# Kernel optimization log

Measured on AMD Instinct MI355X. Metric: run time of the kernel, lower is better.

## Reference

```python
import jax, jax.numpy as jnp
import numpy as np

B, H, N, C = 1024, 768, 100000, 42
LABELED_WEIGHT = 0.7
NUM_LABELED = 100000  # used verbatim in (1 - num_labeled) per the original source
EPS = 1e-8  # F.cosine_similarity default eps


def setup_inputs() -> dict:
    key = jax.random.key(0)
    k1, k2, k3, k4 = jax.random.split(key, 4)
    return {
        "weak_data": jax.random.normal(k1, (B, H), dtype=jnp.float32),
        "weak_logits": jax.random.normal(k2, (B, C), dtype=jnp.float32),
        "labeled_memory": jax.random.normal(k3, (N, H), dtype=jnp.float32),
        "labeled_logits": jax.random.normal(k4, (N, C), dtype=jnp.float32),
    }


def reference(weak_data, weak_logits, labeled_memory, labeled_logits):
    # cosine similarity: normalize rows with eps-clamped norms, then one GEMM
    dn = weak_data / jnp.maximum(jnp.linalg.norm(weak_data, axis=-1, keepdims=True), EPS)
    mn = labeled_memory / jnp.maximum(jnp.linalg.norm(labeled_memory, axis=-1, keepdims=True), EPS)
    sim = jnp.einsum("bh,nh->bn", dn, mn)  # [B, N] similarity (the large intermediate)
    ids = jnp.argmax(sim, axis=1)          # 1-NN index per batch row
    batch_logits = labeled_logits[ids]     # gather [B, C]
    # faithful to source: coefficient is (1 - num_labeled), as written in update_logits
    return batch_logits * LABELED_WEIGHT + (1.0 - NUM_LABELED) * weak_logits
```

## Files before the change

kernel.cpp:

```cpp
#include <hip/hip_runtime.h>
#include <stdint.h>

#define B_ROWS 1024
#define H_DIM  768
#define N_ROWS 100000
#define C_DIM  42
#define NB     64
#define NCHUNK ((N_ROWS + NB - 1) / NB)
#define K2_BLOCKS 782
#define K2_THREADS 512

typedef __attribute__((ext_vector_type(8))) short short8;
typedef __attribute__((ext_vector_type(4))) float f32x4;

__device__ __forceinline__ unsigned short f2bf(float f) {
    union { float f; unsigned u; } x; x.f = f;
    unsigned r = x.u + 0x7FFFu + ((x.u >> 16) & 1u);
    return (unsigned short)(r >> 16);
}

__device__ __forceinline__ unsigned long long packvi(float v, unsigned n) {
    unsigned u = __float_as_uint(v);
    u = (u & 0x80000000u) ? ~u : (u | 0x80000000u);
    return ((unsigned long long)u << 32) | (unsigned long long)(~n);
}

__global__ void k_convA(const float* __restrict__ wd, unsigned short* __restrict__ A) {
    int idx = blockIdx.x * 256 + threadIdx.x;
    float4 v = reinterpret_cast<const float4*>(wd)[idx];
    union { unsigned short s[4]; uint2 u; } o;
    o.s[0] = f2bf(v.x); o.s[1] = f2bf(v.y); o.s[2] = f2bf(v.z); o.s[3] = f2bf(v.w);
    reinterpret_cast<uint2*>(A)[idx] = o.u;
}

__global__ __launch_bounds__(512, 2) void k_simmax(
    const float* __restrict__ mem,
    const unsigned short* __restrict__ A,
    unsigned long long* __restrict__ partial)
{
    __shared__ __align__(16) char ldsB[NB * 1536];
    __shared__ float ldsN[NB];

    const int t    = threadIdx.x;
    const int lane = t & 63;
    const int wv   = t >> 6;
    const int fr   = lane & 15;
    const int kgrp = lane >> 4;

    for (int ci = 0; ci < 2; ++ci) {
        const int c = blockIdx.x + ci * K2_BLOCKS;
        if (c >= NCHUNK) break;
        if (ci) __syncthreads();

        {
            const int r  = t >> 3;
            const int cb = (t & 7) * 4;
            const int n  = c * NB + r;
            const bool valid = (n < N_ROWS);
            const float* src = mem + (long long)n * H_DIM + cb;
            char* dst = ldsB + r * 1536;
            const int sw = (r & 7) << 4;
            float ss = 0.f;
            #pragma unroll
            for (int i = 0; i < 24; ++i) {
                float4 v;
                if (valid) v = *reinterpret_cast<const float4*>(src + i * 32);
                else       v = make_float4(0.f, 0.f, 0.f, 0.f);
                ss += v.x*v.x + v.y*v.y + v.z*v.z + v.w*v.w;
                union { unsigned short s[4]; uint2 u; } o;
                o.s[0]=f2bf(v.x); o.s[1]=f2bf(v.y); o.s[2]=f2bf(v.z); o.s[3]=f2bf(v.w);
                int off = (cb + i * 32) * 2;
                *reinterpret_cast<uint2*>(dst + (off ^ sw)) = o.u;
            }
            ss += __shfl_xor(ss, 1);
            ss += __shfl_xor(ss, 2);
            ss += __shfl_xor(ss, 4);
            if ((t & 7) == 0)
                ldsN[r] = valid ? (1.0f / fmaxf(sqrtf(ss), 1e-8f)) : 0.0f;
        }
        __syncthreads();

        float invn[4];
        #pragma unroll
        for (int nt = 0; nt < 4; ++nt) invn[nt] = ldsN[nt * 16 + fr];

        #pragma unroll
        for (int gi = 0; gi < 2; ++gi) {
            const int b0 = (wv + 8 * gi) * 64;
            f32x4 acc[4][4];
            #pragma unroll
            for (int m = 0; m < 4; ++m)
                #pragma unroll
                for (int n = 0; n < 4; ++n)
                    acc[m][n] = (f32x4){0.f, 0.f, 0.f, 0.f};

            #pragma unroll 4
            for (int k = 0; k < 24; ++k) {
                const int k0 = k * 32 + kgrp * 8;
                short8 af[4], bf[4];
                #pragma unroll
                for (int m = 0; m < 4; ++m) {
                    const unsigned short* ap = A + (b0 + m * 16 + fr) * H_DIM + k0;
                    af[m] = *reinterpret_cast<const short8*>(ap);
                }
                #pragma unroll
                for (int n = 0; n < 4; ++n) {
                    int roww = n * 16 + fr;
                    int off  = roww * 1536 + k0 * 2;
                    off ^= (roww & 7) << 4;
                    bf[n] = *reinterpret_cast<const short8*>(ldsB + off);
                }
                #pragma unroll
                for (int m = 0; m < 4; ++m)
                    #pragma unroll
                    for (int n = 0; n < 4; ++n)
                        acc[m][n] = __builtin_amdgcn_mfma_f32_16x16x32_bf16(af[m], bf[n], acc[m][n], 0, 0, 0);
            }

            #pragma unroll
            for (int m = 0; m < 4; ++m) {
                #pragma unroll
                for (int r = 0; r < 4; ++r) {
                    unsigned long long best = 0ull;
                    #pragma unroll
                    for (int nt = 0; nt < 4; ++nt) {
                        unsigned nglob = (unsigned)(c * NB + nt * 16 + fr);
                        float v = acc[m][nt][r] * invn[nt];
                        unsigned long long p = (nglob < N_ROWS) ? packvi(v, nglob) : 0ull;
                        best = (p > best) ? p : best;
                    }
                    #pragma unroll
                    for (int s = 1; s < 16; s <<= 1) {
                        unsigned long long o = __shfl_xor(best, s);
                        best = (o > best) ? o : best;
                    }
                    if (fr == 0) {
                        int brow = b0 + m * 16 + kgrp * 4 + r;
                        partial[(long long)c * 1024 + brow] = best;
                    }
                }
            }
        }
    }
}

__global__ void k_final(const unsigned long long* __restrict__ partial,
                        const float* __restrict__ wlog,
                        const float* __restrict__ llog,
                        float* __restrict__ out)
{
    __shared__ unsigned long long red[16][17];
    __shared__ int sidx[16];
    const int t  = threadIdx.x;
    const int b0 = blockIdx.x * 16;
    const int i  = t >> 4, j = t & 15;

    unsigned long long best = 0ull;
    for (int c = j; c < NCHUNK; c += 16) {
        unsigned long long p = partial[(long long)c * 1024 + b0 + i];
        best = (p > best) ? p : best;
    }
    red[i][j] = best;
    __syncthreads();
    if (t < 16) {
        unsigned long long m = red[t][0];
        #pragma unroll
        for (int jj = 1; jj < 16; ++jj) { unsigned long long p = red[t][jj]; m = (p > m) ? p : m; }
        sidx[t] = (int)(~(unsigned)(m & 0xFFFFFFFFull));
    }
    __syncthreads();
    for (int e = t; e < 16 * C_DIM; e += 256) {
        int bi = e / C_DIM, cc = e % C_DIM;
        int b  = b0 + bi;
        out[b * C_DIM + cc] = 0.7f * llog[(long long)sidx[bi] * C_DIM + cc]
                            - 99999.0f * wlog[b * C_DIM + cc];
    }
}

extern "C" void kernel_launch(void* const* d_in, const int* in_sizes, int n_in,
                              void* d_out, int out_size, void* d_ws, size_t ws_size,
                              hipStream_t stream) {
    const float* weak_data   = (const float*)d_in[0];
    const float* weak_logits = (const float*)d_in[1];
    const float* mem         = (const float*)d_in[2];
    const float* llog        = (const float*)d_in[3];
    float* out = (float*)d_out;

    unsigned short*     A       = (unsigned short*)d_ws;
    unsigned long long* partial = (unsigned long long*)((char*)d_ws + (2u << 20));

    k_convA <<<768, 256, 0, stream>>>(weak_data, A);
    k_simmax<<<K2_BLOCKS, K2_THREADS, 0, stream>>>(mem, A, partial);
    k_final <<<64, 256, 0, stream>>>(partial, weak_logits, llog, out);
}
```

Measured before the change: 922.8 us.

## Use persistent atomic work queue with register-resident argmax and pre-tiled A layout

Result: faster. 901.6 us (-2.3%).

```diff
diff --git a/kernel.cpp b/kernel.cpp
--- a/kernel.cpp
+++ b/kernel.cpp
@@ -5,10 +5,9 @@
 #define H_DIM  768
 #define N_ROWS 100000
 #define C_DIM  42
-#define NB     64
-#define NCHUNK ((N_ROWS + NB - 1) / NB)
-#define K2_BLOCKS 782
-#define K2_THREADS 512
+#define NB     32
+#define NCHUNK (N_ROWS / NB)
+#define GX     384
 
 typedef __attribute__((ext_vector_type(8))) short short8;
 typedef __attribute__((ext_vector_type(4))) float f32x4;
@@ -25,123 +24,143 @@
     return ((unsigned long long)u << 32) | (unsigned long long)(~n);
 }
 
-__global__ void k_convA(const float* __restrict__ wd, unsigned short* __restrict__ A) {
+__global__ void k_convA(const float* __restrict__ wd, unsigned short* __restrict__ A2,
+                        unsigned int* __restrict__ counters) {
+    if (blockIdx.x == 0 && threadIdx.x == 0) { counters[0] = 0; counters[1] = 0; }
     int idx = blockIdx.x * 256 + threadIdx.x;
+    int row = idx / 192;
+    int c4  = idx - row * 192;
+    int col = c4 * 4;
     float4 v = reinterpret_cast<const float4*>(wd)[idx];
     union { unsigned short s[4]; uint2 u; } o;
     o.s[0] = f2bf(v.x); o.s[1] = f2bf(v.y); o.s[2] = f2bf(v.z); o.s[3] = f2bf(v.w);
-    reinterpret_cast<uint2*>(A)[idx] = o.u;
-}
-
-__global__ __launch_bounds__(512, 2) void k_simmax(
+    size_t byte = (size_t)(((row >> 4) * 96 + (col >> 3)) * 256 + (row & 15) * 16 + (col & 7) * 2);
+    *reinterpret_cast<uint2*>((char*)A2 + byte) = o.u;
+}
+
+__global__ __launch_bounds__(256, 3) void k_simmax(
     const float* __restrict__ mem,
-    const unsigned short* __restrict__ A,
+    const unsigned short* __restrict__ A2,
+    unsigned int* __restrict__ counters,
     unsigned long long* __restrict__ partial)
 {
     __shared__ __align__(16) char ldsB[NB * 1536];
     __shared__ float ldsN[NB];
+    __shared__ int s_c;
 
     const int t    = threadIdx.x;
     const int lane = t & 63;
     const int wv   = t >> 6;
     const int fr   = lane & 15;
     const int kgrp = lane >> 4;
-
-    for (int ci = 0; ci < 2; ++ci) {
-        const int c = blockIdx.x + ci * K2_BLOCKS;
+    const int y    = blockIdx.y;
+
+    float    bv[2][4][4];
+    unsigned bi[2][4][4];
+    #pragma unroll
+    for (int gi = 0; gi < 2; ++gi)
+        #pragma unroll
+        for (int m = 0; m < 4; ++m)
+            #pragma unroll
+            for (int r = 0; r < 4; ++r) { bv[gi][m][r] = -1e30f; bi[gi][m][r] = 0u; }
+
+    const char* A2c = (const char*)A2 + (size_t)lane * 16;
+
+    while (true) {
+        __syncthreads();
+        if (t == 0) s_c = (int)atomicAdd(&counters[y], 1u);
+        __syncthreads();
+        const int c = s_c;
         if (c >= NCHUNK) break;
-        if (ci) __syncthreads();
 
         {
             const int r  = t >> 3;
-            const int cb = (t & 7) * 4;
-            const int n  = c * NB + r;
-            const bool valid = (n < N_ROWS);
-            const float* src = mem + (long long)n * H_DIM + cb;
+            const int j  = t & 7;
+            const float* src = mem + (c * NB + r) * H_DIM + j * 4;
             char* dst = ldsB + r * 1536;
             const int sw = (r & 7) << 4;
             float ss = 0.f;
             #pragma unroll
             for (int i = 0; i < 24; ++i) {
-                float4 v;
-                if (valid) v = *reinterpret_cast<const float4*>(src + i * 32);
-                else       v = make_float4(0.f, 0.f, 0.f, 0.f);
+                float4 v = *reinterpret_cast<const float4*>(src + i * 32);
                 ss += v.x*v.x + v.y*v.y + v.z*v.z + v.w*v.w;
                 union { unsigned short s[4]; uint2 u; } o;
                 o.s[0]=f2bf(v.x); o.s[1]=f2bf(v.y); o.s[2]=f2bf(v.z); o.s[3]=f2bf(v.w);
-                int off = (cb + i * 32) * 2;
-                *reinterpret_cast<uint2*>(dst + (off ^ sw)) = o.u;
+                *reinterpret_cast<uint2*>(dst + ((j * 8 + i * 64) ^ sw)) = o.u;
             }
             ss += __shfl_xor(ss, 1);
             ss += __shfl_xor(ss, 2);
             ss += __shfl_xor(ss, 4);
-            if ((t & 7) == 0)
-                ldsN[r] = valid ? (1.0f / fmaxf(sqrtf(ss), 1e-8f)) : 0.0f;
+            if (j == 0) ldsN[r] = 1.0f / fmaxf(sqrtf(ss), 1e-8f);
         }
         __syncthreads();
 
-        float invn[4];
-        #pragma unroll
-        for (int nt = 0; nt < 4; ++nt) invn[nt] = ldsN[nt * 16 + fr];
+        const float invn[2] = { ldsN[fr], ldsN[16 + fr] };
 
         #pragma unroll
         for (int gi = 0; gi < 2; ++gi) {
-            const int b0 = (wv + 8 * gi) * 64;
-            f32x4 acc[4][4];
+            const int rg0 = y * 32 + gi * 16 + wv * 4;
+            const char* ap = A2c + (size_t)rg0 * 24576;
+            f32x4 acc[4][2];
             #pragma unroll
             for (int m = 0; m < 4; ++m)
                 #pragma unroll
-                for (int n = 0; n < 4; ++n)
-                    acc[m][n] = (f32x4){0.f, 0.f, 0.f, 0.f};
-
-            #pragma unroll 4
+                for (int nt = 0; nt < 2; ++nt)
+                    acc[m][nt] = (f32x4){0.f, 0.f, 0.f, 0.f};
+
+            #pragma unroll 6
             for (int k = 0; k < 24; ++k) {
-                const int k0 = k * 32 + kgrp * 8;
-                short8 af[4], bf[4];
-                #pragma unroll
-                for (int m = 0; m < 4; ++m) {
-                    const unsigned short* ap = A + (b0 + m * 16 + fr) * H_DIM + k0;
-                    af[m] = *reinterpret_cast<const short8*>(ap);
-                }
-                #pragma unroll
-                for (int n = 0; n < 4; ++n) {
-                    int roww = n * 16 + fr;
-                    int off  = roww * 1536 + k0 * 2;
-                    off ^= (roww & 7) << 4;
-                    bf[n] = *reinterpret_cast<const short8*>(ldsB + off);
+                short8 af[4], bfr[2];
+                #pragma unroll
+                for (int m = 0; m < 4; ++m)
+                    af[m] = *reinterpret_cast<const short8*>(ap + m * 24576 + k * 1024);
+                #pragma unroll
+                for (int nt = 0; nt < 2; ++nt) {
+                    int roww = nt * 16 + fr;
+                    int off  = (roww * 1536 + k * 64 + kgrp * 16) ^ ((roww & 7) << 4);
+                    bfr[nt] = *reinterpret_cast<const short8*>(ldsB + off);
                 }
                 #pragma unroll
                 for (int m = 0; m < 4; ++m)
                     #pragma unroll
-                    for (int n = 0; n < 4; ++n)
-                        acc[m][n] = __builtin_amdgcn_mfma_f32_16x16x32_bf16(af[m], bf[n], acc[m][n], 0, 0, 0);
-            }
-
-            #pragma unroll
-            for (int m = 0; m < 4; ++m) {
-                #pragma unroll
-                for (int r = 0; r < 4; ++r) {
-                    unsigned long long best = 0ull;
+                    for (int nt = 0; nt < 2; ++nt)
+                        acc[m][nt] = __builtin_amdgcn_mfma_f32_16x16x32_bf16(af[m], bfr[nt], acc[m][nt], 0, 0, 0);
+            }
+
+            const unsigned nb0 = (unsigned)(c * NB) + (unsigned)fr;
+            #pragma unroll
+            for (int nt = 0; nt < 2; ++nt) {
+                const unsigned nv = nb0 + nt * 16;
+                #pragma unroll
+                for (int m = 0; m < 4; ++m)
                     #pragma unroll
-                    for (int nt = 0; nt < 4; ++nt) {
-                        unsigned nglob = (unsigned)(c * NB + nt * 16 + fr);
+                    for (int r = 0; r < 4; ++r) {
                         float v = acc[m][nt][r] * invn[nt];
-                        unsigned long long p = (nglob < N_ROWS) ? packvi(v, nglob) : 0ull;
-                        best = (p > best) ? p : best;
+                        bool p = v > bv[gi][m][r];
+                        bv[gi][m][r] = p ? v : bv[gi][m][r];
+                        bi[gi][m][r] = p ? nv : bi[gi][m][r];
                     }
-                    #pragma unroll
-                    for (int s = 1; s < 16; s <<= 1) {
-                        unsigned long long o = __shfl_xor(best, s);
-                        best = (o > best) ? o : best;
-                    }
-                    if (fr == 0) {
-                        int brow = b0 + m * 16 + kgrp * 4 + r;
-                        partial[(long long)c * 1024 + brow] = best;
-                    }
+            }
+        }
+    }
+
+    #pragma unroll
+    for (int gi = 0; gi < 2; ++gi)
+        #pragma unroll
+        for (int m = 0; m < 4; ++m)
+            #pragma unroll
+            for (int r = 0; r < 4; ++r) {
+                unsigned long long P = packvi(bv[gi][m][r], bi[gi][m][r]);
+                #pragma unroll
+                for (int s = 1; s < 16; s <<= 1) {
+                    unsigned long long o = __shfl_xor(P, s);
+                    P = (o > P) ? o : P;
                 }
-            }
-        }
-    }
+                if (fr == 0) {
+                    int lb = gi * 256 + wv * 64 + m * 16 + kgrp * 4 + r;
+                    partial[((size_t)y * GX + blockIdx.x) * 512 + lb] = P;
+                }
+            }
 }
 
 __global__ void k_final(const unsigned long long* __restrict__ partial,
@@ -149,31 +168,33 @@
                         const float* __restrict__ llog,
                         float* __restrict__ out)
 {
-    __shared__ unsigned long long red[16][17];
     __shared__ int sidx[16];
     const int t  = threadIdx.x;
     const int b0 = blockIdx.x * 16;
     const int i  = t >> 4, j = t & 15;
 
-    unsigned long long best = 0ull;
-    for (int c = j; c < NCHUNK; c += 16) {
-        unsigned long long p = partial[(long long)c * 1024 + b0 + i];
-        best = (p > best) ? p : best;
-    }
-    red[i][j] = best;
+    const int b  = b0 + i;
+    const int yy = b >> 9;
+    const int lb = b & 511;
+
+    unsigned long long P = 0ull;
+    for (int g = j; g < GX; g += 16) {
+        unsigned long long p = partial[((size_t)yy * GX + g) * 512 + lb];
+        P = (p > P) ? p : P;
+    }
+    #pragma unroll
+    for (int s = 1; s < 16; s <<= 1) {
+        unsigned long long o = __shfl_xor(P, s);
+        P = (o > P) ? o : P;
+    }
+    if (j == 0) sidx[i] = (int)(~(unsigned)(P & 0xFFFFFFFFull));
     __syncthreads();
-    if (t < 16) {
-        unsigned long long m = red[t][0];
-        #pragma unroll
-        for (int jj = 1; jj < 16; ++jj) { unsigned long long p = red[t][jj]; m = (p > m) ? p : m; }
-        sidx[t] = (int)(~(unsigned)(m & 0xFFFFFFFFull));
-    }
-    __syncthreads();
+
     for (int e = t; e < 16 * C_DIM; e += 256) {
-        int bi = e / C_DIM, cc = e % C_DIM;
-        int b  = b0 + bi;
-        out[b * C_DIM + cc] = 0.7f * llog[(long long)sidx[bi] * C_DIM + cc]
-                            - 99999.0f * wlog[b * C_DIM + cc];
+        int bi_ = e / C_DIM, cc = e - bi_ * C_DIM;
+        int bb  = b0 + bi_;
+        out[bb * C_DIM + cc] = 0.7f * llog[(size_t)sidx[bi_] * C_DIM + cc]
+                             - 99999.0f * wlog[bb * C_DIM + cc];
     }
 }
 
@@ -186,10 +207,11 @@
     const float* llog        = (const float*)d_in[3];
     float* out = (float*)d_out;
 
-    unsigned short*     A       = (unsigned short*)d_ws;
-    unsigned long long* partial = (unsigned long long*)((char*)d_ws + (2u << 20));
-
-    k_convA <<<768, 256, 0, stream>>>(weak_data, A);
-    k_simmax<<<K2_BLOCKS, K2_THREADS, 0, stream>>>(mem, A, partial);
+    unsigned short*     A2       = (unsigned short*)d_ws;
+    unsigned int*       counters = (unsigned int*)((char*)d_ws + 0x180000);
+    unsigned long long* partial  = (unsigned long long*)((char*)d_ws + 0x200000);
+
+    k_convA <<<768, 256, 0, stream>>>(weak_data, A2, counters);
+    k_simmax<<<dim3(GX, 2), 256, 0, stream>>>(mem, A2, counters, partial);
     k_final <<<64, 256, 0, stream>>>(partial, weak_logits, llog, out);
 }
```
